# Optimization experiments

Hardware: AMD Instinct MI355X
Metric: run time of the kernel (lower is better)

Reference implementation:

```python
import jax, jax.numpy as jnp
import numpy as np
import math

N = 100000      # num nodes
D = 5           # fixed degree per node (<=5 -> exact Shapley enumeration path)
F_IN = 128
F_OUT = 128


def _subset_coeffs(d):
    """Exact Shapley subset-enumeration coefficients for a node with d neighbors.
    For subset S (mask m_k over neighbor slots, |S|=s):
      marginal = (sum_S + x_i)/(s+1) - (sum_S/s if s>0 else 0)   [since mean_S]
      weight   = s! (d-s)! / (d+1)!
    contrib = sum_k w_k*marginal_k = einsum(sum_S, c1) + x_i * sum(c2)
    """
    k = np.arange(2 ** d)
    masks = ((k[:, None] >> np.arange(d)) & 1).astype(np.float32)  # [2^d, d]
    s = masks.sum(axis=1)
    fact = np.vectorize(math.factorial)
    w = (fact(s.astype(np.int64)) * fact((d - s).astype(np.int64))
         / math.factorial(d + 1)).astype(np.float32)
    c1 = np.where(s > 0, w * (1.0 / (s + 1.0) - 1.0 / np.maximum(s, 1.0)), 0.0).astype(np.float32)
    c2 = (w / (s + 1.0)).astype(np.float32)
    return jnp.asarray(masks), jnp.asarray(c1), jnp.asarray(float(c2.sum()))


def setup_inputs() -> dict:
    key = jax.random.key(0)
    k1, k2, k3 = jax.random.split(key, 3)
    x = jax.random.normal(k1, (N, F_IN), dtype=jnp.float32)
    # fixed-degree graph: node i owns edges [i*D, (i+1)*D); row sorted
    row = jnp.repeat(jnp.arange(N, dtype=jnp.int32), D)
    col = jax.random.randint(k2, (N * D,), 0, N, dtype=jnp.int32)
    edge_index = jnp.stack([row, col])  # [2, N*D]
    W = jax.random.normal(k3, (F_OUT, F_IN), dtype=jnp.float32) / np.float32(np.sqrt(F_IN))
    return {"x": x, "edge_index": edge_index, "W": W}


def reference(x, edge_index, W):
    n = x.shape[0]
    col = edge_index[1]
    d = col.shape[0] // n
    nbrs = col.reshape(n, d)          # neighbors of node i (row is sorted, fixed degree)
    xn = x[nbrs]                      # [n, d, f] gathered neighbor features
    masks, c1, c2_sum = _subset_coeffs(d)
    # per-subset neighbor-feature sums: [n, 2^d, f]
    sum_S = jnp.einsum('kd,ndf->nkf', masks, xn)
    contrib = jnp.einsum('nkf,k->nf', sum_S, c1) + x * c2_sum
    shapley = x + contrib             # x_i + Shapley contribution
    out = jax.nn.relu(shapley @ W.T)  # Linear(bias=False) + relu
    return out
```

## Files before the change

kernel.cpp:

```cpp
#include <hip/hip_runtime.h>
#include <hip/hip_bf16.h>

typedef __attribute__((ext_vector_type(8))) short short8;
typedef __attribute__((ext_vector_type(4))) float f32x4;

#define DEG 5
#define FDIM 128
#define MT 32
#define NTHR 256
#define LROW 136
#define NBG 625

#define CSELF 1.4083333333333334f
#define ALPHA (-0.04833333333333333f)

__device__ __forceinline__ short f2bf(float f) {
    unsigned u = __builtin_bit_cast(unsigned, f);
    unsigned r = (u + 0x7fffu + ((u >> 16) & 1u)) >> 16;
    return (short)(r & 0xffffu);
}
__device__ __forceinline__ float bf2f(short s) {
    return __builtin_bit_cast(float, (unsigned)((unsigned short)s) << 16);
}

__global__ __launch_bounds__(256) void prep_w_kernel(
    const float* __restrict__ W, short* __restrict__ wswz)
{
    int t = blockIdx.x * 256 + threadIdx.x;
    int frag = t >> 6;
    int lane = t & 63;
    int tt = frag >> 2;
    int kk = frag & 3;
    int lr = lane & 15;
    int lg = lane >> 4;
    const float4* wp = reinterpret_cast<const float4*>(W + (tt * 16 + lr) * FDIM + kk * 32 + lg * 8);
    float4 w0 = wp[0], w1 = wp[1];
    short8 v;
    v[0] = f2bf(w0.x); v[1] = f2bf(w0.y); v[2] = f2bf(w0.z); v[3] = f2bf(w0.w);
    v[4] = f2bf(w1.x); v[5] = f2bf(w1.y); v[6] = f2bf(w1.z); v[7] = f2bf(w1.w);
    *reinterpret_cast<short8*>(wswz + (size_t)t * 8) = v;
}

__global__ __launch_bounds__(256) void conv_xb_kernel(
    const float* __restrict__ x, short* __restrict__ xb, long total8)
{
    long t = (long)blockIdx.x * 256 + threadIdx.x;
    if (t < total8) {
        const f32x4* xp = reinterpret_cast<const f32x4*>(x + t * 8);
        f32x4 a = xp[0], b = xp[1];
        short8 v;
        v[0] = f2bf(a[0]); v[1] = f2bf(a[1]); v[2] = f2bf(a[2]); v[3] = f2bf(a[3]);
        v[4] = f2bf(b[0]); v[5] = f2bf(b[1]); v[6] = f2bf(b[2]); v[7] = f2bf(b[3]);
        *reinterpret_cast<short8*>(xb + t * 8) = v;
    }
}

struct SetRegs {
    short8 self[2];
    short8 nb[2][DEG];
    int tbase;
    int valid;
};

__device__ __forceinline__ void load_tile(
    SetRegs& S, int tt, int NT,
    const short* __restrict__ xb, const int* __restrict__ col,
    int n, int tid)
{
    S.valid = (tt < NT);
    int tb = (S.valid ? tt : 0) * MT;
    S.tbase = tb;
    const int c = tid & 15;
    const int srow = tid >> 4;
    #pragma unroll
    for (int u = 0; u < 2; ++u) {
        int node = tb + u * 16 + srow;
        int nc = node < n ? node : 0;
        S.self[u] = *reinterpret_cast<const short8*>(xb + (size_t)nc * FDIM + c * 8);
        #pragma unroll
        for (int j = 0; j < DEG; ++j) {
            int nbr = col[nc * DEG + j];
            S.nb[u][j] = *reinterpret_cast<const short8*>(xb + (size_t)nbr * FDIM + c * 8);
        }
    }
}

__device__ __forceinline__ void comp_tile(
    const SetRegs& S, short* sS,
    const short* __restrict__ wswz, float* __restrict__ out,
    int n, int tid)
{
    const int c = tid & 15;
    const int srow = tid >> 4;

    #pragma unroll
    for (int u = 0; u < 2; ++u) {
        int row = u * 16 + srow;
        short8 v;
        #pragma unroll
        for (int k = 0; k < 8; ++k) {
            float s = bf2f(S.nb[u][0][k]) + bf2f(S.nb[u][1][k]) + bf2f(S.nb[u][2][k])
                    + bf2f(S.nb[u][3][k]) + bf2f(S.nb[u][4][k]);
            float vf = CSELF * bf2f(S.self[u][k]) + ALPHA * s;
            v[k] = f2bf(vf);
        }
        *reinterpret_cast<short8*>(&sS[row * LROW + c * 8]) = v;
    }
    __syncthreads();

    const int wave = tid >> 6;
    const int lane = tid & 63;
    const int lr = lane & 15;
    const int lg = lane >> 4;
    const int rt = wave & 1;
    const int cg = wave >> 1;

    short8 af[4];
    const short* arow = &sS[(rt * 16 + lr) * LROW];
    #pragma unroll
    for (int kk = 0; kk < 4; ++kk)
        af[kk] = *reinterpret_cast<const short8*>(arow + kk * 32 + lg * 8);
    __syncthreads();

    f32x4 acc[4];
    #pragma unroll
    for (int q = 0; q < 4; ++q) acc[q] = (f32x4){0.f, 0.f, 0.f, 0.f};

    #pragma unroll
    for (int q = 0; q < 4; ++q) {
        int tcol = cg * 4 + q;
        #pragma unroll
        for (int kk = 0; kk < 4; ++kk) {
            short8 bf = *reinterpret_cast<const short8*>(
                wswz + (((size_t)(tcol * 4 + kk) * 64 + lane) * 8));
            acc[q] = __builtin_amdgcn_mfma_f32_16x16x32_bf16(af[kk], bf, acc[q], 0, 0, 0);
        }
    }

    #pragma unroll
    for (int q = 0; q < 4; ++q) {
        #pragma unroll
        for (int i = 0; i < 4; ++i) {
            int nrow = S.tbase + rt * 16 + lg * 4 + i;
            if (nrow < n) {
                float v = acc[q][i];
                out[(size_t)nrow * FDIM + (cg * 4 + q) * 16 + lr] = v > 0.f ? v : 0.f;
            }
        }
    }
}

__global__ __launch_bounds__(NTHR) void shapley_persistent_kernel(
    const short* __restrict__ xb,
    const int* __restrict__ col,
    const short* __restrict__ wswz,
    float* __restrict__ out,
    int n, int NT)
{
    __shared__ short sS[MT * LROW];
    const int tid = threadIdx.x;
    const int b = blockIdx.x;
    const int G = gridDim.x;

    SetRegs A, B;
    load_tile(A, b, NT, xb, col, n, tid);
    int k = 0;
    while (true) {
        load_tile(B, b + (k + 1) * G, NT, xb, col, n, tid);
        if (A.valid) comp_tile(A, sS, wswz, out, n, tid);
        ++k;
        if (b + (size_t)k * G >= (size_t)NT) break;
        load_tile(A, b + (k + 1) * G, NT, xb, col, n, tid);
        if (B.valid) comp_tile(B, sS, wswz, out, n, tid);
        ++k;
        if (b + (size_t)k * G >= (size_t)NT) break;
    }
}

__global__ __launch_bounds__(NTHR) void shapley_fb_kernel(
    const float* __restrict__ x,
    const int* __restrict__ col,
    const short* __restrict__ wswz,
    float* __restrict__ out,
    int n)
{
    __shared__ short sS[64 * LROW];
    __shared__ int sIdx[64 * DEG];

    const int tid = threadIdx.x;
    const int base = blockIdx.x * 64;

    for (int i = tid; i < 64 * DEG; i += NTHR) {
        int e = base * DEG + i;
        sIdx[i] = (e < n * DEG) ? col[e] : 0;
    }
    __syncthreads();

    for (int t = tid; t < 64 * 16; t += NTHR) {
        int m = t >> 4;
        int c = t & 15;
        int node = base + m;
        float a0, a1, a2, a3, a4, a5, a6, a7;
        if (node < n) {
            const float4* xp = reinterpret_cast<const float4*>(x + (size_t)node * FDIM + c * 8);
            float4 s0 = xp[0], s1 = xp[1];
            a0 = CSELF * s0.x; a1 = CSELF * s0.y; a2 = CSELF * s0.z; a3 = CSELF * s0.w;
            a4 = CSELF * s1.x; a5 = CSELF * s1.y; a6 = CSELF * s1.z; a7 = CSELF * s1.w;
            #pragma unroll
            for (int j = 0; j < DEG; ++j) {
                int nb = sIdx[m * DEG + j];
                const float4* np = reinterpret_cast<const float4*>(x + (size_t)nb * FDIM + c * 8);
                float4 b0 = np[0], b1 = np[1];
                a0 += ALPHA * b0.x; a1 += ALPHA * b0.y; a2 += ALPHA * b0.z; a3 += ALPHA * b0.w;
                a4 += ALPHA * b1.x; a5 += ALPHA * b1.y; a6 += ALPHA * b1.z; a7 += ALPHA * b1.w;
            }
        } else {
            a0 = a1 = a2 = a3 = a4 = a5 = a6 = a7 = 0.f;
        }
        short8 v;
        v[0] = f2bf(a0); v[1] = f2bf(a1); v[2] = f2bf(a2); v[3] = f2bf(a3);
        v[4] = f2bf(a4); v[5] = f2bf(a5); v[6] = f2bf(a6); v[7] = f2bf(a7);
        *reinterpret_cast<short8*>(&sS[m * LROW + c * 8]) = v;
    }
    __syncthreads();

    const int wave = tid >> 6;
    const int lane = tid & 63;
    const int lr = lane & 15;
    const int lg = lane >> 4;

    short8 afrag[4];
    const short* arow = &sS[(wave * 16 + lr) * LROW];
    #pragma unroll
    for (int kk = 0; kk < 4; ++kk)
        afrag[kk] = *reinterpret_cast<const short8*>(arow + kk * 32 + lg * 8);

    f32x4 acc[8];
    #pragma unroll
    for (int t = 0; t < 8; ++t) acc[t] = (f32x4){0.f, 0.f, 0.f, 0.f};

    #pragma unroll
    for (int t = 0; t < 8; ++t) {
        #pragma unroll
        for (int kk = 0; kk < 4; ++kk) {
            short8 bfrag = *reinterpret_cast<const short8*>(
                wswz + (((size_t)(t * 4 + kk) * 64 + lane) * 8));
            acc[t] = __builtin_amdgcn_mfma_f32_16x16x32_bf16(afrag[kk], bfrag, acc[t], 0, 0, 0);
        }
    }

    #pragma unroll
    for (int t = 0; t < 8; ++t) {
        #pragma unroll
        for (int i = 0; i < 4; ++i) {
            int nrow = base + wave * 16 + lg * 4 + i;
            if (nrow < n) {
                float v = acc[t][i];
                out[(size_t)nrow * FDIM + t * 16 + lr] = v > 0.f ? v : 0.f;
            }
        }
    }
}

extern "C" void kernel_launch(void* const* d_in, const int* in_sizes, int n_in,
                              void* d_out, int out_size, void* d_ws, size_t ws_size,
                              hipStream_t stream) {
    const float* x  = (const float*)d_in[0];
    const int* ei   = (const int*)d_in[1];
    const float* W  = (const float*)d_in[2];
    float* out      = (float*)d_out;

    int n = in_sizes[0] / FDIM;
    const int* col = ei + (size_t)n * DEG;

    short* wswz = (short*)d_ws;
    size_t xb_off = 32768;
    size_t need   = xb_off + (size_t)n * FDIM * sizeof(short);

    hipLaunchKernelGGL(prep_w_kernel, dim3(8), dim3(256), 0, stream, W, wswz);

    if (ws_size >= need) {
        short* xb = (short*)((char*)d_ws + xb_off);
        long total8 = (long)n * FDIM / 8;
        int cblocks = (int)((total8 + 255) / 256);
        hipLaunchKernelGGL(conv_xb_kernel, dim3(cblocks), dim3(256), 0, stream,
                           x, xb, total8);
        int NT = (n + MT - 1) / MT;
        int g = NT < NBG ? NT : NBG;
        hipLaunchKernelGGL(shapley_persistent_kernel, dim3(g), dim3(NTHR), 0, stream,
                           xb, col, wswz, out, n, NT);
    } else {
        int blocks = (n + 63) / 64;
        hipLaunchKernelGGL(shapley_fb_kernel, dim3(blocks), dim3(NTHR), 0, stream,
                           x, col, wswz, out, n);
    }
}
```

Baseline: 56.89 us.

## Replace persistent double-buffered kernel with per-wave gather directly into MFMA fragments

The persistent, double-buffered tile kernel that staged combined features through shared memory with two barriers per tile is replaced by a non-persistent kernel. In the new kernel each wave handles 16 nodes and each lane gathers the self and neighbor features already laid out as MFMA A fragments. All 128 output columns are computed per wave with no LDS or __syncthreads. This removes the shared-memory round trip and block barriers and exposes more parallelism through many more blocks. In exchange it raises register pressure, since each lane holds 24 short8 values, and drops the explicit software prefetch across tiles.

Result: slower. 61.22 us (+7.6%).

```diff
diff --git a/kernel.cpp b/kernel.cpp
--- a/kernel.cpp
+++ b/kernel.cpp
@@ -6,10 +6,8 @@
 
 #define DEG 5
 #define FDIM 128
-#define MT 32
 #define NTHR 256
 #define LROW 136
-#define NBG 625
 
 #define CSELF 1.4083333333333334f
 #define ALPHA (-0.04833333333333333f)
@@ -55,125 +53,80 @@
     }
 }
 
-struct SetRegs {
-    short8 self[2];
-    short8 nb[2][DEG];
-    int tbase;
-    int valid;
-};
-
-__device__ __forceinline__ void load_tile(
-    SetRegs& S, int tt, int NT,
-    const short* __restrict__ xb, const int* __restrict__ col,
-    int n, int tid)
-{
-    S.valid = (tt < NT);
-    int tb = (S.valid ? tt : 0) * MT;
-    S.tbase = tb;
-    const int c = tid & 15;
-    const int srow = tid >> 4;
-    #pragma unroll
-    for (int u = 0; u < 2; ++u) {
-        int node = tb + u * 16 + srow;
-        int nc = node < n ? node : 0;
-        S.self[u] = *reinterpret_cast<const short8*>(xb + (size_t)nc * FDIM + c * 8);
-        #pragma unroll
-        for (int j = 0; j < DEG; ++j) {
-            int nbr = col[nc * DEG + j];
-            S.nb[u][j] = *reinterpret_cast<const short8*>(xb + (size_t)nbr * FDIM + c * 8);
-        }
-    }
-}
-
-__device__ __forceinline__ void comp_tile(
-    const SetRegs& S, short* sS,
-    const short* __restrict__ wswz, float* __restrict__ out,
-    int n, int tid)
-{
-    const int c = tid & 15;
-    const int srow = tid >> 4;
-
-    #pragma unroll
-    for (int u = 0; u < 2; ++u) {
-        int row = u * 16 + srow;
-        short8 v;
-        #pragma unroll
-        for (int k = 0; k < 8; ++k) {
-            float s = bf2f(S.nb[u][0][k]) + bf2f(S.nb[u][1][k]) + bf2f(S.nb[u][2][k])
-                    + bf2f(S.nb[u][3][k]) + bf2f(S.nb[u][4][k]);
-            float vf = CSELF * bf2f(S.self[u][k]) + ALPHA * s;
-            v[k] = f2bf(vf);
-        }
-        *reinterpret_cast<short8*>(&sS[row * LROW + c * 8]) = v;
-    }
-    __syncthreads();
-
-    const int wave = tid >> 6;
-    const int lane = tid & 63;
-    const int lr = lane & 15;
-    const int lg = lane >> 4;
-    const int rt = wave & 1;
-    const int cg = wave >> 1;
-
-    short8 af[4];
-    const short* arow = &sS[(rt * 16 + lr) * LROW];
-    #pragma unroll
-    for (int kk = 0; kk < 4; ++kk)
-        af[kk] = *reinterpret_cast<const short8*>(arow + kk * 32 + lg * 8);
-    __syncthreads();
-
-    f32x4 acc[4];
-    #pragma unroll
-    for (int q = 0; q < 4; ++q) acc[q] = (f32x4){0.f, 0.f, 0.f, 0.f};
-
-    #pragma unroll
-    for (int q = 0; q < 4; ++q) {
-        int tcol = cg * 4 + q;
-        #pragma unroll
-        for (int kk = 0; kk < 4; ++kk) {
-            short8 bf = *reinterpret_cast<const short8*>(
-                wswz + (((size_t)(tcol * 4 + kk) * 64 + lane) * 8));
-            acc[q] = __builtin_amdgcn_mfma_f32_16x16x32_bf16(af[kk], bf, acc[q], 0, 0, 0);
-        }
-    }
-
-    #pragma unroll
-    for (int q = 0; q < 4; ++q) {
-        #pragma unroll
-        for (int i = 0; i < 4; ++i) {
-            int nrow = S.tbase + rt * 16 + lg * 4 + i;
-            if (nrow < n) {
-                float v = acc[q][i];
-                out[(size_t)nrow * FDIM + (cg * 4 + q) * 16 + lr] = v > 0.f ? v : 0.f;
-            }
-        }
-    }
-}
-
-__global__ __launch_bounds__(NTHR) void shapley_persistent_kernel(
+__global__ __launch_bounds__(NTHR) void shapley_gather_kernel(
     const short* __restrict__ xb,
     const int* __restrict__ col,
     const short* __restrict__ wswz,
     float* __restrict__ out,
-    int n, int NT)
-{
-    __shared__ short sS[MT * LROW];
+    int n)
+{
     const int tid = threadIdx.x;
-    const int b = blockIdx.x;
-    const int G = gridDim.x;
-
-    SetRegs A, B;
-    load_tile(A, b, NT, xb, col, n, tid);
-    int k = 0;
-    while (true) {
-        load_tile(B, b + (k + 1) * G, NT, xb, col, n, tid);
-        if (A.valid) comp_tile(A, sS, wswz, out, n, tid);
-        ++k;
-        if (b + (size_t)k * G >= (size_t)NT) break;
-        load_tile(A, b + (k + 1) * G, NT, xb, col, n, tid);
-        if (B.valid) comp_tile(B, sS, wswz, out, n, tid);
-        ++k;
-        if (b + (size_t)k * G >= (size_t)NT) break;
+    const int wave = tid >> 6;
+    const int lane = tid & 63;
+    const int r = lane & 15;
+    const int h = lane >> 4;
+
+    const int grp = blockIdx.x * 4 + wave;
+    const int node = grp * 16 + r;
+    const int nc = node < n ? node : 0;
+
+    int idx[DEG];
+    #pragma unroll
+    for (int j = 0; j < DEG; ++j) idx[j] = col[nc * DEG + j];
+
+    short8 self[4];
+    short8 nb[DEG][4];
+    {
+        const short* sp = xb + (size_t)nc * FDIM + h * 8;
+        #pragma unroll
+        for (int kk = 0; kk < 4; ++kk)
+            self[kk] = *reinterpret_cast<const short8*>(sp + kk * 32);
+        #pragma unroll
+        for (int j = 0; j < DEG; ++j) {
+            const short* np = xb + (size_t)idx[j] * FDIM + h * 8;
+            #pragma unroll
+            for (int kk = 0; kk < 4; ++kk)
+                nb[j][kk] = *reinterpret_cast<const short8*>(np + kk * 32);
+        }
+    }
+    __builtin_amdgcn_sched_barrier(0);
+
+    short8 af[4];
+    #pragma unroll
+    for (int kk = 0; kk < 4; ++kk) {
+        #pragma unroll
+        for (int e = 0; e < 8; ++e) {
+            float s = bf2f(nb[0][kk][e]) + bf2f(nb[1][kk][e]) + bf2f(nb[2][kk][e])
+                    + bf2f(nb[3][kk][e]) + bf2f(nb[4][kk][e]);
+            float v = CSELF * bf2f(self[kk][e]) + ALPHA * s;
+            af[kk][e] = f2bf(v);
+        }
+    }
+
+    f32x4 acc[8];
+    #pragma unroll
+    for (int q = 0; q < 8; ++q) acc[q] = (f32x4){0.f, 0.f, 0.f, 0.f};
+
+    #pragma unroll
+    for (int q = 0; q < 8; ++q) {
+        #pragma unroll
+        for (int kk = 0; kk < 4; ++kk) {
+            short8 bf = *reinterpret_cast<const short8*>(
+                wswz + (((size_t)(q * 4 + kk) * 64 + lane) * 8));
+            acc[q] = __builtin_amdgcn_mfma_f32_16x16x32_bf16(af[kk], bf, acc[q], 0, 0, 0);
+        }
+    }
+
+    #pragma unroll
+    for (int q = 0; q < 8; ++q) {
+        #pragma unroll
+        for (int i = 0; i < 4; ++i) {
+            int orow = grp * 16 + h * 4 + i;
+            if (orow < n) {
+                float v = acc[q][i];
+                out[(size_t)orow * FDIM + q * 16 + r] = v > 0.f ? v : 0.f;
+            }
+        }
     }
 }
 
@@ -285,10 +238,10 @@
         int cblocks = (int)((total8 + 255) / 256);
         hipLaunchKernelGGL(conv_xb_kernel, dim3(cblocks), dim3(256), 0, stream,
                            x, xb, total8);
-        int NT = (n + MT - 1) / MT;
-        int g = NT < NBG ? NT : NBG;
-        hipLaunchKernelGGL(shapley_persistent_kernel, dim3(g), dim3(NTHR), 0, stream,
-                           xb, col, wswz, out, n, NT);
+        int groups = (n + 15) / 16;
+        int blocks = (groups + 3) / 4;
+        hipLaunchKernelGGL(shapley_gather_kernel, dim3(blocks), dim3(NTHR), 0, stream,
+                           xb, col, wswz, out, n);
     } else {
         int blocks = (n + 63) / 64;
         hipLaunchKernelGGL(shapley_fb_kernel, dim3(blocks), dim3(NTHR), 0, stream,
```
